# Performance work log

Hardware: AMD Instinct MI355X
Metric: run time of the kernel (lower is better)

The kernel has to match this reference:

```python
import jax, jax.numpy as jnp
import numpy as np

N_NODES = 100000
N_EDGES = 1600000
F_IN = 128
HIDDEN = 128
N_CLASSES = 2
N_GRAPHS = 512


def setup_inputs() -> dict:
    key = jax.random.key(0)
    ks = jax.random.split(key, 10)
    node_features = jax.random.normal(ks[0], (N_NODES, F_IN), dtype=jnp.float32)
    edge_index = jax.random.randint(ks[1], (2, N_EDGES), 0, N_NODES, dtype=jnp.int64)
    batch = jnp.sort(jax.random.randint(ks[2], (N_NODES,), 0, N_GRAPHS, dtype=jnp.int64))
    s1 = 1.0 / np.sqrt(F_IN)
    s2 = 1.0 / np.sqrt(HIDDEN)
    W1 = jax.random.uniform(ks[3], (F_IN, HIDDEN), jnp.float32, -s1, s1)
    b1 = jnp.zeros((HIDDEN,), jnp.float32)
    W2 = jax.random.uniform(ks[4], (HIDDEN, HIDDEN), jnp.float32, -s2, s2)
    b2 = jnp.zeros((HIDDEN,), jnp.float32)
    Wlin = jax.random.uniform(ks[5], (HIDDEN, N_CLASSES), jnp.float32, -s2, s2)
    blin = jax.random.uniform(ks[6], (N_CLASSES,), jnp.float32, -s2, s2)
    return {"node_features": node_features, "edge_index": edge_index, "batch": batch,
            "W1": W1, "b1": b1, "W2": W2, "b2": b2, "Wlin": Wlin, "blin": blin}


def _gcn_conv(x, src, dst, norm, W, b, n_nodes):
    # transform-then-propagate (PyG GCNConv default)
    h = x @ W                                   # [N, H]
    msg = h[src] * norm[:, None]                # gather + edge scale
    out = jax.ops.segment_sum(msg, dst, num_segments=n_nodes)  # scatter-add
    return out + b


def reference(node_features, edge_index, batch, W1, b1, W2, b2, Wlin, blin):
    n = node_features.shape[0]
    loop = jnp.arange(n, dtype=edge_index.dtype)
    src = jnp.concatenate([edge_index[0], loop])  # add self-loops
    dst = jnp.concatenate([edge_index[1], loop])
    # symmetric degree normalization: deg counts incoming edges incl. self-loop
    deg = jax.ops.segment_sum(jnp.ones_like(src, dtype=node_features.dtype), dst, num_segments=n)
    dis = jnp.where(deg > 0, jax.lax.rsqrt(jnp.maximum(deg, 1.0)), 0.0)
    norm = dis[src] * dis[dst]

    x = jax.nn.relu(_gcn_conv(node_features, src, dst, norm, W1, b1, n))
    x = jax.nn.relu(_gcn_conv(x, src, dst, norm, W2, b2, n))

    # global mean pool over graphs
    ones = jnp.ones((n,), dtype=x.dtype)
    counts = jax.ops.segment_sum(ones, batch, num_segments=N_GRAPHS)
    sums = jax.ops.segment_sum(x, batch, num_segments=N_GRAPHS)
    pooled = sums / jnp.maximum(counts, 1.0)[:, None]

    # dropout is identity in eval mode
    return pooled @ Wlin + blin
```

## Files before the change

kernel.cpp:

```cpp
#include <hip/hip_runtime.h>
#include <hip/hip_bf16.h>
#include <hip/hip_fp16.h>

constexpr int NN = 100000;
constexpr int NE = 1600000;
constexpr int NG = 512;
constexpr int F  = 128;

constexpr int NB   = 392;
constexpr int RCAP = 4608;
constexpr int CAP  = 32;

typedef _Float16 f16;
typedef f16 f16x2 __attribute__((ext_vector_type(2)));
typedef f16 f16x4 __attribute__((ext_vector_type(4)));
typedef f16 f16x8 __attribute__((ext_vector_type(8)));
typedef float f32x4 __attribute__((ext_vector_type(4)));
typedef unsigned int u32;
typedef u32 u32x4a __attribute__((ext_vector_type(4), aligned(4)));

__global__ void init_cursors(int* __restrict__ gcur) {
    int b = blockIdx.x * blockDim.x + threadIdx.x;
    if (b < NB) gcur[b] = b * RCAP;
}

__global__ __launch_bounds__(256) void bin_edges(const int* __restrict__ ei,
                                                 int* __restrict__ gcur,
                                                 u32* __restrict__ binned) {
    __shared__ u32 stage[NB][CAP];
    __shared__ int scnt[NB];
    for (int b = threadIdx.x; b < NB; b += 256) scnt[b] = 0;
    __syncthreads();
    const int per = NE / 256;
    const int e0 = blockIdx.x * per;
    for (int r = 0; r < per; r += 256) {
        int k = r + threadIdx.x;
        if (k < per) {
            int e = e0 + k;
            int s = ei[e], d = ei[NE + e];
            int b = d >> 8;
            u32 v = ((u32)(d & 255) << 24) | (u32)s;
            int p = atomicAdd(&scnt[b], 1);
            if (p < CAP) stage[b][p] = v;
        }
        __syncthreads();
        for (int b2 = threadIdx.x; b2 < NB; b2 += 256) {
            int n = scnt[b2];
            if (n >= 16) {
                int f = n & ~15;
                int base = atomicAdd(&gcur[b2], f);
                const u32x4a* st4 = (const u32x4a*)&stage[b2][0];
                u32x4a* out4 = (u32x4a*)&binned[base];
                for (int j = 0; j < (f >> 2); j++) out4[j] = st4[j];
                for (int j = 0; j < n - f; j++) stage[b2][j] = stage[b2][f + j];
                scnt[b2] = n - f;
            }
        }
        __syncthreads();
    }
    for (int b2 = threadIdx.x; b2 < NB; b2 += 256) {
        int n = scnt[b2];
        if (n > 0) {
            int base = atomicAdd(&gcur[b2], n);
            for (int j = 0; j < n; j++) binned[base + j] = stage[b2][j];
        }
    }
}

__global__ void scan_buckets(const int* __restrict__ gcur, int* __restrict__ bucketBase,
                             int* __restrict__ offs) {
    __shared__ int tmp[512];
    int t = threadIdx.x;
    int c = (t < NB) ? (gcur[t] - t * RCAP) : 0;
    tmp[t] = c;
    __syncthreads();
    for (int d = 1; d < 512; d <<= 1) {
        int x = (t >= d) ? tmp[t - d] : 0;
        __syncthreads();
        tmp[t] += x;
        __syncthreads();
    }
    if (t < NB) bucketBase[t] = tmp[t] - c;
    if (t == 0) offs[NN] = NE;
}

__global__ __launch_bounds__(256) void build_csr(const u32* __restrict__ binned,
                                                 const int* __restrict__ gcur,
                                                 const int* __restrict__ bucketBase,
                                                 int* __restrict__ offs,
                                                 float* __restrict__ dis,
                                                 int* __restrict__ csr_src) {
    __shared__ u32 ed[RCAP];
    __shared__ u32 lcsr[RCAP];
    __shared__ int hist[256];
    __shared__ int loff[256];
    __shared__ int lcur[256];
    const int b = blockIdx.x;
    int cnt = gcur[b] - b * RCAP;
    if (cnt > RCAP) cnt = RCAP;
    const int gbase = bucketBase[b];
    const int t = threadIdx.x;
    hist[t] = 0;
    __syncthreads();
    for (int j = t; j < cnt; j += 256) {
        u32 v = binned[(size_t)b * RCAP + j];
        ed[j] = v;
        atomicAdd(&hist[v >> 24], 1);
    }
    __syncthreads();
    int h = hist[t];
    loff[t] = h;
    __syncthreads();
    for (int d = 1; d < 256; d <<= 1) {
        int x = (t >= d) ? loff[t - d] : 0;
        __syncthreads();
        loff[t] += x;
        __syncthreads();
    }
    int excl = loff[t] - h;
    lcur[t] = excl;
    int node = (b << 8) + t;
    if (node < NN) {
        offs[node] = gbase + excl;
        dis[node] = rsqrtf((float)(h + 1));
    }
    __syncthreads();
    for (int j = t; j < cnt; j += 256) {
        u32 v = ed[j];
        int p = atomicAdd(&lcur[v >> 24], 1);
        lcsr[p] = v & 0x1FFFFu;
    }
    __syncthreads();
    for (int j = t; j < cnt; j += 256) csr_src[gbase + j] = (int)lcsr[j];
}

__global__ void prep_w(const float* __restrict__ W1, const float* __restrict__ W2,
                       f16* __restrict__ WT1, f16* __restrict__ WT2) {
    int idx = blockIdx.x * blockDim.x + threadIdx.x;
    if (idx < 128 * 128) {
        int n = idx >> 7, k = idx & 127;
        WT1[idx] = (f16)W1[k * 128 + n];
        WT2[idx] = (f16)W2[k * 128 + n];
    }
}

template<bool IN_HALF>
__global__ __launch_bounds__(256) void gemm_mfma(const void* __restrict__ Xv,
                                                 const f16* __restrict__ WT,
                                                 const float* __restrict__ dis,
                                                 f16* __restrict__ H, int M) {
    __shared__ f16 sX[128 * 136];
    __shared__ f16 sW[128 * 136];
    const int tid = threadIdx.x;
    const int row0 = blockIdx.x * 128;
    {
        const f16x8* Wg = (const f16x8*)WT;
        #pragma unroll
        for (int i = 0; i < 8; i++) {
            int idx = tid + 256 * i;
            int n = idx >> 4, kc = idx & 15;
            *(f16x8*)&sW[n * 136 + kc * 8] = Wg[idx];
        }
    }
    if (IN_HALF) {
        const f16x8* Xg = (const f16x8*)Xv;
        #pragma unroll
        for (int i = 0; i < 8; i++) {
            int idx = tid + 256 * i;
            int r = idx >> 4, kc = idx & 15;
            f16x8 v = {};
            if (row0 + r < M) v = Xg[(size_t)(row0 + r) * 16 + kc];
            *(f16x8*)&sX[r * 136 + kc * 8] = v;
        }
    } else {
        const float4* Xg = (const float4*)Xv;
        #pragma unroll
        for (int i = 0; i < 16; i++) {
            int idx = tid + 256 * i;
            int r = idx >> 5, c4 = idx & 31;
            float4 v = make_float4(0.f, 0.f, 0.f, 0.f);
            if (row0 + r < M) v = Xg[(size_t)(row0 + r) * 32 + c4];
            f16x4 hv = {(f16)v.x, (f16)v.y, (f16)v.z, (f16)v.w};
            *(f16x4*)&sX[r * 136 + c4 * 4] = hv;
        }
    }
    __syncthreads();

    const int wid = tid >> 6;
    const int lane = tid & 63;
    const int wrow = wid * 32;
    const int lr = lane & 15;
    const int lk = (lane >> 4) * 8;
    f32x4 acc[2][8] = {};
    #pragma unroll
    for (int ks = 0; ks < 4; ks++) {
        f16x8 a[2], b[8];
        #pragma unroll
        for (int mf = 0; mf < 2; mf++)
            a[mf] = *(const f16x8*)&sX[(wrow + mf * 16 + lr) * 136 + ks * 32 + lk];
        #pragma unroll
        for (int nf = 0; nf < 8; nf++)
            b[nf] = *(const f16x8*)&sW[(nf * 16 + lr) * 136 + ks * 32 + lk];
        #pragma unroll
        for (int mf = 0; mf < 2; mf++)
            #pragma unroll
            for (int nf = 0; nf < 8; nf++)
                acc[mf][nf] = __builtin_amdgcn_mfma_f32_16x16x32_f16(a[mf], b[nf], acc[mf][nf], 0, 0, 0);
    }
    const int crow = (lane >> 4) * 4;
    #pragma unroll
    for (int mf = 0; mf < 2; mf++) {
        #pragma unroll
        for (int reg = 0; reg < 4; reg++) {
            int row = row0 + wrow + mf * 16 + crow + reg;
            if (row < M) {
                float sc = dis[row];
                #pragma unroll
                for (int nf = 0; nf < 8; nf++)
                    H[(size_t)row * 128 + nf * 16 + lr] = (f16)(acc[mf][nf][reg] * sc);
            }
        }
    }
}

__global__ __launch_bounds__(256) void aggregate16(const f16* __restrict__ h,
                                                   const int* __restrict__ offs,
                                                   const int* __restrict__ csr_src,
                                                   const float* __restrict__ dis,
                                                   const float* __restrict__ bias,
                                                   f16* __restrict__ out, int n) {
    int i = blockIdx.x * 4 + (threadIdx.x >> 6);
    if (i >= n) return;
    const int lane = threadIdx.x & 63;
    const int q = lane >> 4;
    const int r = lane & 15;
    float acc[8] = {};
    if (q == 0) {
        f16x8 v = *(const f16x8*)(h + (size_t)i * F + r * 8);
        #pragma unroll
        for (int j = 0; j < 8; j++) acc[j] = (float)v[j];
    }
    const int s = offs[i], e = offs[i + 1];
    int t = s + q;
    for (; t + 4 < e; t += 8) {
        int sr0 = csr_src[t];
        int sr1 = csr_src[t + 4];
        f16x8 v0 = *(const f16x8*)(h + (size_t)sr0 * F + r * 8);
        f16x8 v1 = *(const f16x8*)(h + (size_t)sr1 * F + r * 8);
        #pragma unroll
        for (int j = 0; j < 8; j++) acc[j] += (float)v0[j] + (float)v1[j];
    }
    if (t < e) {
        int sr = csr_src[t];
        f16x8 v = *(const f16x8*)(h + (size_t)sr * F + r * 8);
        #pragma unroll
        for (int j = 0; j < 8; j++) acc[j] += (float)v[j];
    }
    #pragma unroll
    for (int j = 0; j < 8; j++) {
        acc[j] += __shfl_xor(acc[j], 16);
        acc[j] += __shfl_xor(acc[j], 32);
    }
    if (q == 0) {
        float di = dis[i];
        const float4* b4 = (const float4*)bias;
        float4 bb0 = b4[r * 2], bb1 = b4[r * 2 + 1];
        float bb[8] = {bb0.x, bb0.y, bb0.z, bb0.w, bb1.x, bb1.y, bb1.z, bb1.w};
        f16x8 o;
        #pragma unroll
        for (int j = 0; j < 8; j++) {
            float v = fmaf(acc[j], di, bb[j]);
            o[j] = (f16)(v > 0.f ? v : 0.f);
        }
        *(f16x8*)(out + (size_t)i * F + r * 8) = o;
    }
}

__global__ __launch_bounds__(128) void pool_linear(const f16* __restrict__ x,
                                                   const int* __restrict__ batch,
                                                   const float* __restrict__ Wlin,
                                                   const float* __restrict__ blin,
                                                   float* __restrict__ out, int n) {
    int g = blockIdx.x;
    int f = threadIdx.x;
    __shared__ int se[2];
    if (threadIdx.x < 2) {
        int target = g + threadIdx.x;
        int lo = 0, hi = n;
        while (lo < hi) {
            int mid = (lo + hi) >> 1;
            if (batch[mid] < target) lo = mid + 1; else hi = mid;
        }
        se[threadIdx.x] = lo;
    }
    __syncthreads();
    int s = se[0], e = se[1];
    float acc = 0.f;
    for (int i = s; i < e; i++) acc += (float)x[(size_t)i * F + f];
    float cnt = (float)((e - s) > 0 ? (e - s) : 1);
    float p = acc / cnt;
    float v0 = p * Wlin[f * 2 + 0];
    float v1 = p * Wlin[f * 2 + 1];
    #pragma unroll
    for (int o = 32; o > 0; o >>= 1) {
        v0 += __shfl_xor(v0, o);
        v1 += __shfl_xor(v1, o);
    }
    __shared__ float red[4];
    int wid = threadIdx.x >> 6;
    if ((threadIdx.x & 63) == 0) { red[wid * 2] = v0; red[wid * 2 + 1] = v1; }
    __syncthreads();
    if (threadIdx.x == 0) {
        out[g * 2 + 0] = red[0] + red[2] + blin[0];
        out[g * 2 + 1] = red[1] + red[3] + blin[1];
    }
}

extern "C" void kernel_launch(void* const* d_in, const int* in_sizes, int n_in,
                              void* d_out, int out_size, void* d_ws, size_t ws_size,
                              hipStream_t stream) {
    const float* X     = (const float*)d_in[0];
    const int*   ei    = (const int*)d_in[1];
    const int*   batch = (const int*)d_in[2];
    const float* W1    = (const float*)d_in[3];
    const float* b1    = (const float*)d_in[4];
    const float* W2    = (const float*)d_in[5];
    const float* b2    = (const float*)d_in[6];
    const float* Wlin  = (const float*)d_in[7];
    const float* blin  = (const float*)d_in[8];
    float* out = (float*)d_out;

    char* p = (char*)d_ws;
    auto alloc = [&](size_t bytes) -> char* {
        char* r = p;
        p += (bytes + 255) & ~size_t(255);
        return r;
    };
    int*   gcur       = (int*)alloc((size_t)NB * 4);
    int*   bucketBase = (int*)alloc((size_t)NB * 4);
    int*   offs       = (int*)alloc((size_t)(NN + 1) * 4);
    float* dis        = (float*)alloc((size_t)NN * 4);
    u32*   binned     = (u32*)alloc((size_t)NB * RCAP * 4);
    int*   csr_src    = (int*)alloc((size_t)NE * 4);
    f16*   WT1        = (f16*)alloc((size_t)128 * 128 * 2);
    f16*   WT2        = (f16*)alloc((size_t)128 * 128 * 2);
    f16*   bufA       = (f16*)alloc((size_t)NN * F * 2);
    f16*   bufB       = (f16*)alloc((size_t)NN * F * 2);

    init_cursors<<<2, 256, 0, stream>>>(gcur);
    bin_edges<<<256, 256, 0, stream>>>(ei, gcur, binned);
    scan_buckets<<<1, 512, 0, stream>>>(gcur, bucketBase, offs);
    build_csr<<<NB, 256, 0, stream>>>(binned, gcur, bucketBase, offs, dis, csr_src);
    prep_w<<<64, 256, 0, stream>>>(W1, W2, WT1, WT2);

    gemm_mfma<false><<<(NN + 127) / 128, 256, 0, stream>>>(X, WT1, dis, bufA, NN);
    aggregate16<<<(NN + 3) / 4, 256, 0, stream>>>(bufA, offs, csr_src, dis, b1, bufB, NN);
    gemm_mfma<true><<<(NN + 127) / 128, 256, 0, stream>>>(bufB, WT2, dis, bufA, NN);
    aggregate16<<<(NN + 3) / 4, 256, 0, stream>>>(bufA, offs, csr_src, dis, b2, bufB, NN);
    pool_linear<<<NG, 128, 0, stream>>>(bufB, batch, Wlin, blin, out, NN);
}
```

Measured before the change: 315.2 us.

## Fuse second aggregation with mean-pool via atomics and merge init into weight prep

Fuses the second GCN aggregation with the graph pooling. Each block reduces its four nodes' ReLU outputs into shared memory and atomically adds them into a per-graph float accumulator, so the second layer's output is never written out and re-read by a serial per-graph loop. The cursor init is folded into the weight-prep kernel, the edge gather loop is unrolled to four rows per iteration, and nontemporal loads are used for the edge streams. The cost is a memset plus many global float atomics, which makes the pooled sums order-nondeterministic.

```diff
diff --git a/kernel.cpp b/kernel.cpp
--- a/kernel.cpp
+++ b/kernel.cpp
@@ -19,9 +19,16 @@
 typedef unsigned int u32;
 typedef u32 u32x4a __attribute__((ext_vector_type(4), aligned(4)));
 
-__global__ void init_cursors(int* __restrict__ gcur) {
-    int b = blockIdx.x * blockDim.x + threadIdx.x;
-    if (b < NB) gcur[b] = b * RCAP;
+__global__ void prep_w(const float* __restrict__ W1, const float* __restrict__ W2,
+                       f16* __restrict__ WT1, f16* __restrict__ WT2,
+                       int* __restrict__ gcur) {
+    int idx = blockIdx.x * blockDim.x + threadIdx.x;
+    if (idx < NB) gcur[idx] = idx * RCAP;
+    if (idx < 128 * 128) {
+        int n = idx >> 7, k = idx & 127;
+        WT1[idx] = (f16)W1[k * 128 + n];
+        WT2[idx] = (f16)W2[k * 128 + n];
+    }
 }
 
 __global__ __launch_bounds__(256) void bin_edges(const int* __restrict__ ei,
@@ -37,7 +44,8 @@
         int k = r + threadIdx.x;
         if (k < per) {
             int e = e0 + k;
-            int s = ei[e], d = ei[NE + e];
+            int s = __builtin_nontemporal_load(&ei[e]);
+            int d = __builtin_nontemporal_load(&ei[NE + e]);
             int b = d >> 8;
             u32 v = ((u32)(d & 255) << 24) | (u32)s;
             int p = atomicAdd(&scnt[b], 1);
@@ -103,7 +111,7 @@
     hist[t] = 0;
     __syncthreads();
     for (int j = t; j < cnt; j += 256) {
-        u32 v = binned[(size_t)b * RCAP + j];
+        u32 v = __builtin_nontemporal_load(&binned[(size_t)b * RCAP + j]);
         ed[j] = v;
         atomicAdd(&hist[v >> 24], 1);
     }
@@ -132,16 +140,6 @@
     }
     __syncthreads();
     for (int j = t; j < cnt; j += 256) csr_src[gbase + j] = (int)lcsr[j];
-}
-
-__global__ void prep_w(const float* __restrict__ W1, const float* __restrict__ W2,
-                       f16* __restrict__ WT1, f16* __restrict__ WT2) {
-    int idx = blockIdx.x * blockDim.x + threadIdx.x;
-    if (idx < 128 * 128) {
-        int n = idx >> 7, k = idx & 127;
-        WT1[idx] = (f16)W1[k * 128 + n];
-        WT2[idx] = (f16)W2[k * 128 + n];
-    }
 }
 
 template<bool IN_HALF>
@@ -220,6 +218,43 @@
                     H[(size_t)row * 128 + nf * 16 + lr] = (f16)(acc[mf][nf][reg] * sc);
             }
         }
+    }
+}
+
+__device__ __forceinline__ void gather_rows(const f16* __restrict__ h, int i,
+                                            const int* __restrict__ offs,
+                                            const int* __restrict__ csr_src,
+                                            int q, int r, float acc[8]) {
+    if (q == 0) {
+        f16x8 v = *(const f16x8*)(h + (size_t)i * F + r * 8);
+        #pragma unroll
+        for (int j = 0; j < 8; j++) acc[j] = (float)v[j];
+    }
+    const int s = offs[i], e = offs[i + 1];
+    int t = s + q;
+    for (; t + 12 < e; t += 16) {
+        int sr0 = __builtin_nontemporal_load(&csr_src[t]);
+        int sr1 = __builtin_nontemporal_load(&csr_src[t + 4]);
+        int sr2 = __builtin_nontemporal_load(&csr_src[t + 8]);
+        int sr3 = __builtin_nontemporal_load(&csr_src[t + 12]);
+        f16x8 v0 = *(const f16x8*)(h + (size_t)sr0 * F + r * 8);
+        f16x8 v1 = *(const f16x8*)(h + (size_t)sr1 * F + r * 8);
+        f16x8 v2 = *(const f16x8*)(h + (size_t)sr2 * F + r * 8);
+        f16x8 v3 = *(const f16x8*)(h + (size_t)sr3 * F + r * 8);
+        #pragma unroll
+        for (int j = 0; j < 8; j++)
+            acc[j] += ((float)v0[j] + (float)v1[j]) + ((float)v2[j] + (float)v3[j]);
+    }
+    for (; t < e; t += 4) {
+        int sr = __builtin_nontemporal_load(&csr_src[t]);
+        f16x8 v = *(const f16x8*)(h + (size_t)sr * F + r * 8);
+        #pragma unroll
+        for (int j = 0; j < 8; j++) acc[j] += (float)v[j];
+    }
+    #pragma unroll
+    for (int j = 0; j < 8; j++) {
+        acc[j] += __shfl_xor(acc[j], 16);
+        acc[j] += __shfl_xor(acc[j], 32);
     }
 }
 
@@ -235,32 +270,7 @@
     const int q = lane >> 4;
     const int r = lane & 15;
     float acc[8] = {};
-    if (q == 0) {
-        f16x8 v = *(const f16x8*)(h + (size_t)i * F + r * 8);
-        #pragma unroll
-        for (int j = 0; j < 8; j++) acc[j] = (float)v[j];
-    }
-    const int s = offs[i], e = offs[i + 1];
-    int t = s + q;
-    for (; t + 4 < e; t += 8) {
-        int sr0 = csr_src[t];
-        int sr1 = csr_src[t + 4];
-        f16x8 v0 = *(const f16x8*)(h + (size_t)sr0 * F + r * 8);
-        f16x8 v1 = *(const f16x8*)(h + (size_t)sr1 * F + r * 8);
-        #pragma unroll
-        for (int j = 0; j < 8; j++) acc[j] += (float)v0[j] + (float)v1[j];
-    }
-    if (t < e) {
-        int sr = csr_src[t];
-        f16x8 v = *(const f16x8*)(h + (size_t)sr * F + r * 8);
-        #pragma unroll
-        for (int j = 0; j < 8; j++) acc[j] += (float)v[j];
-    }
-    #pragma unroll
-    for (int j = 0; j < 8; j++) {
-        acc[j] += __shfl_xor(acc[j], 16);
-        acc[j] += __shfl_xor(acc[j], 32);
-    }
+    gather_rows(h, i, offs, csr_src, q, r, acc);
     if (q == 0) {
         float di = dis[i];
         const float4* b4 = (const float4*)bias;
@@ -276,11 +286,66 @@
     }
 }
 
-__global__ __launch_bounds__(128) void pool_linear(const f16* __restrict__ x,
-                                                   const int* __restrict__ batch,
-                                                   const float* __restrict__ Wlin,
-                                                   const float* __restrict__ blin,
-                                                   float* __restrict__ out, int n) {
+__global__ __launch_bounds__(256) void aggregate_pool(const f16* __restrict__ h,
+                                                      const int* __restrict__ offs,
+                                                      const int* __restrict__ csr_src,
+                                                      const float* __restrict__ dis,
+                                                      const float* __restrict__ bias,
+                                                      const int* __restrict__ batch,
+                                                      float* __restrict__ partial, int n) {
+    const int wid = threadIdx.x >> 6;
+    const int lane = threadIdx.x & 63;
+    int i = blockIdx.x * 4 + wid;
+    const bool valid = i < n;
+    const int ii = valid ? i : (n - 1);
+    const int q = lane >> 4;
+    const int r = lane & 15;
+    float acc[8] = {};
+    gather_rows(h, ii, offs, csr_src, q, r, acc);
+    __shared__ float sacc[4][128];
+    __shared__ int sg[4];
+    if (q == 0) {
+        float di = dis[ii];
+        const float4* b4 = (const float4*)bias;
+        float4 bb0 = b4[r * 2], bb1 = b4[r * 2 + 1];
+        float bb[8] = {bb0.x, bb0.y, bb0.z, bb0.w, bb1.x, bb1.y, bb1.z, bb1.w};
+        #pragma unroll
+        for (int j = 0; j < 8; j++) {
+            float v = fmaf(acc[j], di, bb[j]);
+            v = v > 0.f ? v : 0.f;
+            sacc[wid][r * 8 + j] = valid ? v : 0.f;
+        }
+    }
+    if (lane == 0) sg[wid] = valid ? batch[ii] : -1;
+    __syncthreads();
+    if (wid == 0) {
+        const int f0 = lane * 2, f1 = lane * 2 + 1;
+        int g0 = sg[0], g1 = sg[1], g2 = sg[2], g3 = sg[3];
+        if (g0 == g1 && g1 == g2 && g2 == g3) {
+            if (g0 >= 0) {
+                float s0 = (sacc[0][f0] + sacc[1][f0]) + (sacc[2][f0] + sacc[3][f0]);
+                float s1 = (sacc[0][f1] + sacc[1][f1]) + (sacc[2][f1] + sacc[3][f1]);
+                atomicAdd(&partial[(size_t)g0 * F + f0], s0);
+                atomicAdd(&partial[(size_t)g0 * F + f1], s1);
+            }
+        } else {
+            #pragma unroll
+            for (int w = 0; w < 4; w++) {
+                int g = sg[w];
+                if (g >= 0) {
+                    atomicAdd(&partial[(size_t)g * F + f0], sacc[w][f0]);
+                    atomicAdd(&partial[(size_t)g * F + f1], sacc[w][f1]);
+                }
+            }
+        }
+    }
+}
+
+__global__ __launch_bounds__(128) void pool_final(const float* __restrict__ partial,
+                                                  const int* __restrict__ batch,
+                                                  const float* __restrict__ Wlin,
+                                                  const float* __restrict__ blin,
+                                                  float* __restrict__ out, int n) {
     int g = blockIdx.x;
     int f = threadIdx.x;
     __shared__ int se[2];
@@ -295,10 +360,8 @@
     }
     __syncthreads();
     int s = se[0], e = se[1];
-    float acc = 0.f;
-    for (int i = s; i < e; i++) acc += (float)x[(size_t)i * F + f];
     float cnt = (float)((e - s) > 0 ? (e - s) : 1);
-    float p = acc / cnt;
+    float p = partial[(size_t)g * F + f] / cnt;
     float v0 = p * Wlin[f * 2 + 0];
     float v1 = p * Wlin[f * 2 + 1];
     #pragma unroll
@@ -346,16 +409,17 @@
     f16*   WT2        = (f16*)alloc((size_t)128 * 128 * 2);
     f16*   bufA       = (f16*)alloc((size_t)NN * F * 2);
     f16*   bufB       = (f16*)alloc((size_t)NN * F * 2);
-
-    init_cursors<<<2, 256, 0, stream>>>(gcur);
+    float* partial    = (float*)alloc((size_t)NG * F * 4);
+
+    prep_w<<<64, 256, 0, stream>>>(W1, W2, WT1, WT2, gcur);
     bin_edges<<<256, 256, 0, stream>>>(ei, gcur, binned);
     scan_buckets<<<1, 512, 0, stream>>>(gcur, bucketBase, offs);
     build_csr<<<NB, 256, 0, stream>>>(binned, gcur, bucketBase, offs, dis, csr_src);
-    prep_w<<<64, 256, 0, stream>>>(W1, W2, WT1, WT2);
+    hipMemsetAsync(partial, 0, (size_t)NG * F * 4, stream);
 
     gemm_mfma<false><<<(NN + 127) / 128, 256, 0, stream>>>(X, WT1, dis, bufA, NN);
     aggregate16<<<(NN + 3) / 4, 256, 0, stream>>>(bufA, offs, csr_src, dis, b1, bufB, NN);
     gemm_mfma<true><<<(NN + 127) / 128, 256, 0, stream>>>(bufB, WT2, dis, bufA, NN);
-    aggregate16<<<(NN + 3) / 4, 256, 0, stream>>>(bufA, offs, csr_src, dis, b2, bufB, NN);
-    pool_linear<<<NG, 128, 0, stream>>>(bufB, batch, Wlin, blin, out, NN);
-}
+    aggregate_pool<<<(NN + 3) / 4, 256, 0, stream>>>(bufA, offs, csr_src, dis, b2, batch, partial, NN);
+    pool_final<<<NG, 128, 0, stream>>>(partial, batch, Wlin, blin, out, NN);
+}
```

New measurement: 281.9 us. -10.6%, faster.
